# Optimization experiments

Measured on AMD Instinct MI355X. Metric: run time of the kernel, lower is better.

The kernel has to match this reference:

```python
import jax, jax.numpy as jnp
import numpy as np

N_HEADS, HEAD_D, N_LVL, N_PTS, EMB = 8, 32, 1, 4, 256


def _grid_sample(img, grid):
    """Bilinear grid_sample, align_corners=False, zeros padding.
    img: [N,C,H,W], grid: [N,Hg,Wg,2] in [-1,1] (x=width, y=height)."""
    N, C, H, W = img.shape
    x = (grid[..., 0] + 1.0) * (W * 0.5) - 0.5
    y = (grid[..., 1] + 1.0) * (H * 0.5) - 0.5
    x0 = jnp.floor(x); y0 = jnp.floor(y)
    x1 = x0 + 1.0; y1 = y0 + 1.0
    wx1 = x - x0; wx0 = 1.0 - wx1
    wy1 = y - y0; wy0 = 1.0 - wy1
    img_flat = img.reshape(N, C, H * W)

    def gather(xi, yi, w):
        xii = xi.astype(jnp.int32); yii = yi.astype(jnp.int32)
        valid = (xii >= 0) & (xii < W) & (yii >= 0) & (yii < H)
        lin = jnp.clip(yii, 0, H - 1) * W + jnp.clip(xii, 0, W - 1)   # [N,Hg,Wg]
        vals = jnp.take_along_axis(img_flat, lin.reshape(N, 1, -1), axis=2)
        vals = vals.reshape(N, C, lin.shape[1], lin.shape[2])
        return vals * (w * valid)[:, None]

    return (gather(x0, y0, wx0 * wy0) + gather(x1, y0, wx1 * wy0)
            + gather(x0, y1, wx0 * wy1) + gather(x1, y1, wx1 * wy1))


def setup_inputs() -> dict:
    key = jax.random.key(0)
    ks = jax.random.split(key, 16)
    bs, nq, Hl, Wl = 4, 10000, 100, 100
    nv = Hl * Wl
    s = 0.02
    return {
        "query": jax.random.normal(ks[0], (bs, nq, EMB), jnp.float32),
        "key": jax.random.normal(ks[1], (bs, nv, EMB), jnp.float32),
        "value": jax.random.normal(ks[2], (bs, nv, EMB), jnp.float32),
        "reference_points": jax.random.uniform(ks[3], (bs, nq, N_LVL, 2), jnp.float32),
        "Wq": s * jax.random.normal(ks[4], (HEAD_D, HEAD_D), jnp.float32),
        "bq": jnp.zeros((HEAD_D,), jnp.float32),
        "Wk": s * jax.random.normal(ks[5], (HEAD_D, HEAD_D), jnp.float32),
        "bk": jnp.zeros((HEAD_D,), jnp.float32),
        "Wv": s * jax.random.normal(ks[6], (HEAD_D, HEAD_D), jnp.float32),
        "bv": jnp.zeros((HEAD_D,), jnp.float32),
        "Woff": s * jax.random.normal(ks[7], (N_LVL * N_PTS * 2, HEAD_D), jnp.float32),
        "boff": jnp.zeros((N_LVL * N_PTS * 2,), jnp.float32),
        "Wo": s * jax.random.normal(ks[8], (EMB, EMB), jnp.float32),
        "bo": jnp.zeros((EMB,), jnp.float32),
        "spatial_shapes": jnp.array([[Hl, Wl]], dtype=jnp.int32),
    }


def reference(query, key, value, reference_points, Wq, bq, Wk, bk, Wv, bv,
              Woff, boff, Wo, bo, spatial_shapes):
    nH, D, nL, nP = N_HEADS, HEAD_D, N_LVL, N_PTS
    bs, nq, _ = query.shape
    ss = np.asarray(spatial_shapes)                      # static [L,2] (H,W)
    residual = query
    qh = query.reshape(bs, nq, nH, D)
    kh = key.reshape(bs, -1, nH, D)
    vh = value.reshape(bs, -1, nH, D)
    norm = jnp.asarray(np.stack([ss[:, 1], ss[:, 0]], -1), jnp.float32)  # (W,H) per level
    off = (qh @ Woff.T + boff).reshape(bs, nq, nH, nL, nP, 2)
    loc = reference_points[:, :, None, :, None, :] + off / norm[None, None, None, :, None, :]
    grids = 2.0 * loc - 1.0                              # [b,q,h,L,P,2]
    k_parts, v_parts = [], []
    start = 0
    for l in range(nL):
        Hl, Wl = int(ss[l, 0]), int(ss[l, 1])
        sl = slice(start, start + Hl * Wl); start += Hl * Wl
        k_img = kh[:, sl].reshape(bs, Hl * Wl, nH * D).transpose(0, 2, 1).reshape(bs * nH, D, Hl, Wl)
        v_img = vh[:, sl].reshape(bs, Hl * Wl, nH * D).transpose(0, 2, 1).reshape(bs * nH, D, Hl, Wl)
        # NOTE: key grid uses only the FIRST query's sampling locations (as in source: grids[:, :1])
        gk = grids[:, :1, :, l].transpose(0, 2, 1, 3, 4).reshape(bs * nH, 1, nP, 2)
        gv = grids[:, :, :, l].transpose(0, 2, 1, 3, 4).reshape(bs * nH, nq, nP, 2)
        k_parts.append(_grid_sample(k_img, gk))          # [bH, D, 1, P]
        v_parts.append(_grid_sample(v_img, gv))          # [bH, D, nq, P]
    k_samp = jnp.stack(k_parts, axis=-2).reshape(bs * nH, D, nL * nP)
    k_samp = k_samp.reshape(bs, nH, D, nL * nP).transpose(0, 3, 1, 2)     # [b, LP, h, d]
    v_samp = jnp.stack(v_parts, axis=-2).reshape(bs * nH, D, nq, nL * nP)  # [bH, d, q, LP]
    q = qh @ Wq.T + bq                                                    # [b, q, h, d]
    k = k_samp @ Wk.T + bk                                                # [b, LP, h, d]
    v = (v_samp.transpose(0, 2, 3, 1) @ Wv.T + bv).transpose(0, 3, 1, 2)  # [bH, d, q, LP]
    attn = jax.nn.softmax(jnp.einsum('bqhd,bkhd->bqhk', q, k), axis=-1)   # [b, q, h, LP]
    attn = attn.transpose(0, 2, 1, 3).reshape(bs * nH, 1, nq, nL * nP)
    out = (v * attn).sum(-1).reshape(bs, nH * D, nq).transpose(0, 2, 1)   # [b, q, E]
    return out @ Wo.T + bo + residual  # dropout is identity in eval mode
```

## Files before the change

### kernel.cpp

```cpp
#include <hip/hip_runtime.h>
#include <hip/hip_bf16.h>
#include <math.h>

#define NH   8
#define HD   32
#define NP   4
#define EMB  256
#define IMG_H 100
#define IMG_W 100
#define NQ   10000
#define NV   10000
#define BS   4

#define W4S 36

#define FENCE() asm volatile("" ::: "memory")

typedef __attribute__((ext_vector_type(8))) short bf16x8;
typedef __attribute__((ext_vector_type(4))) float f32x4;

#define KT_OFF    0
#define KB_OFF    16384
#define BO2_OFF   17408
#define WCF_OFF   18432
#define WCB_OFF   (18432 + 262144)
#define PREB_OFF  (18432 + 262144 + 131072)
#define WS_MIN    ((size_t)PREB_OFF)
#define WS_FULL   ((size_t)PREB_OFF + (size_t)BS * NQ * EMB * 2)

__global__ __launch_bounds__(64) void k1_keys(
    const float* __restrict__ query, const float* __restrict__ key,
    const float* __restrict__ refp,  const float* __restrict__ Woff,
    const float* __restrict__ boff,  const float* __restrict__ Wk,
    const float* __restrict__ bk,    const float* __restrict__ Wq,
    const float* __restrict__ bq,
    float* __restrict__ kt, float* __restrict__ kb)
{
    int b = blockIdx.x >> 3, h = blockIdx.x & 7;
    __shared__ float q0[HD];
    __shared__ float off[8];
    __shared__ float ks[NP][HD];
    __shared__ float kkl[NP][HD];
    int l = threadIdx.x;

    if (l < HD) q0[l] = query[(size_t)(b * NQ) * EMB + h * HD + l];
    __syncthreads();

    if (l < 8) {
        float s = boff[l];
        #pragma unroll
        for (int d = 0; d < HD; ++d) s += q0[d] * Woff[l * HD + d];
        off[l] = s;
    }
    __syncthreads();

    if (l < HD) {
        float refx = refp[(size_t)(b * NQ) * 2 + 0];
        float refy = refp[(size_t)(b * NQ) * 2 + 1];
        for (int p = 0; p < NP; ++p) {
            float x = refx * IMG_W + off[p * 2 + 0] - 0.5f;
            float y = refy * IMG_H + off[p * 2 + 1] - 0.5f;
            float x0f = floorf(x), y0f = floorf(y);
            int ix0 = (int)x0f, iy0 = (int)y0f;
            float fx = x - x0f, fy = y - y0f;
            float acc = 0.f;
            #pragma unroll
            for (int cy = 0; cy < 2; ++cy)
                #pragma unroll
                for (int cx = 0; cx < 2; ++cx) {
                    int xi = ix0 + cx, yi = iy0 + cy;
                    if ((unsigned)xi < IMG_W && (unsigned)yi < IMG_H) {
                        float wgt = (cx ? fx : 1.f - fx) * (cy ? fy : 1.f - fy);
                        acc += wgt * key[((size_t)b * NV + yi * IMG_W + xi) * EMB + h * HD + l];
                    }
                }
            ks[p][l] = acc;
        }
    }
    __syncthreads();

    #pragma unroll
    for (int t = 0; t < 2; ++t) {
        int idx = l + 64 * t;
        int p = idx >> 5, dout = idx & 31;
        float s = bk[dout];
        #pragma unroll
        for (int d = 0; d < HD; ++d) s += Wk[dout * HD + d] * ks[p][d];
        kkl[p][dout] = s;
    }
    __syncthreads();

    #pragma unroll
    for (int t = 0; t < 2; ++t) {
        int idx = l + 64 * t;
        int p = idx >> 5, d = idx & 31;
        float s = 0.f;
        #pragma unroll
        for (int dd = 0; dd < HD; ++dd) s += Wq[dd * HD + d] * kkl[p][dd];
        kt[((b * NP + p) * NH + h) * HD + d] = s;
    }
    if (l < NP) {
        float s = 0.f;
        #pragma unroll
        for (int dd = 0; dd < HD; ++dd) s += bq[dd] * kkl[l][dd];
        kb[(b * NP + l) * NH + h] = s;
    }
}

__global__ __launch_bounds__(256) void kcomb(
    const float* __restrict__ Wo, const float* __restrict__ Wv,
    const float* __restrict__ bv, const float* __restrict__ bo,
    float* __restrict__ wcf, __hip_bfloat16* __restrict__ wcb,
    float* __restrict__ bo2)
{
    __shared__ float sWv[HD * HD];
    __shared__ float sWoR[EMB];
    __shared__ float sws[4];
    int e = blockIdx.x, col = threadIdx.x;
    *(float4*)&sWv[col * 4] = *(const float4*)(Wv + col * 4);
    sWoR[col] = Wo[(size_t)e * EMB + col];
    __syncthreads();

    int h = col >> 5, d = col & 31;
    float s = 0.f;
    #pragma unroll
    for (int dd = 0; dd < HD; ++dd) s += sWoR[h * HD + dd] * sWv[dd * HD + d];
    wcf[(size_t)e * EMB + col] = s;
    wcb[(size_t)e * EMB + col] = __float2bfloat16(s);

    float pb = bv[d] * sWoR[col];
    #pragma unroll
    for (int o = 1; o < 64; o <<= 1) pb += __shfl_xor(pb, o);
    if ((col & 63) == 0) sws[col >> 6] = pb;
    __syncthreads();
    if (col == 0) bo2[e] = bo[e] + sws[0] + sws[1] + sws[2] + sws[3];
}

template<int BF16OUT>
__global__ __launch_bounds__(256) void k2_main(
    const float* __restrict__ query, const float* __restrict__ value,
    const float* __restrict__ refp,
    const float* __restrict__ Woff, const float* __restrict__ boff,
    const float* __restrict__ kt, const float* __restrict__ kb,
    float* __restrict__ pre, __hip_bfloat16* __restrict__ preb)
{
    __shared__ float sWoff[8 * W4S];
    __shared__ float sboff[8];
    __shared__ float skt[NP * NH * W4S];
    __shared__ float skb[NP * NH];
    __shared__ float qld[4][NH * W4S];
    __shared__ float offs[4][64];
    __shared__ float attnw[4][32];
    __shared__ int   soff4[4][32][4];
    __shared__ float swgt4[4][32][4];

    int tid = threadIdx.x;
    int b0 = (blockIdx.x * 4) / NQ;

    for (int i = tid; i < 8 * HD; i += 256) sWoff[(i >> 5) * W4S + (i & 31)] = Woff[i];
    if (tid < 8)  sboff[tid] = boff[tid];
    {
        int j = tid * 4;
        *(float4*)&skt[(j >> 5) * W4S + (j & 31)] =
            *(const float4*)(kt + b0 * (NP * NH * HD) + j);
    }
    if (tid < NP * NH) skb[tid] = kb[b0 * (NP * NH) + tid];

    int w = tid >> 6, lane = tid & 63;
    int gq = blockIdx.x * 4 + w;
    int b = b0;

    float4 qv = *(const float4*)(query + (size_t)gq * EMB + lane * 4);
    { int e = lane * 4; *(float4*)&qld[w][(e >> 5) * W4S + (e & 31)] = qv; }
    float refx = refp[(size_t)gq * 2 + 0];
    float refy = refp[(size_t)gq * 2 + 1];
    __syncthreads();

    int h = lane >> 3, t = lane & 7;

    float qr[HD];
    #pragma unroll
    for (int d = 0; d < HD; d += 4) {
        float4 v4 = *(const float4*)&qld[w][h * W4S + d];
        qr[d] = v4.x; qr[d + 1] = v4.y; qr[d + 2] = v4.z; qr[d + 3] = v4.w;
    }

    {
        float s = sboff[t];
        const float* wr = &sWoff[t * W4S];
        #pragma unroll
        for (int d = 0; d < HD; d += 4) {
            float4 ww = *(const float4*)(wr + d);
            s += qr[d] * ww.x + qr[d+1] * ww.y + qr[d+2] * ww.z + qr[d+3] * ww.w;
        }
        offs[w][h * 8 + t] = s;
    }

    float plog[NP];
    #pragma unroll
    for (int p = 0; p < NP; ++p) {
        const float* kr = &skt[(p * NH + h) * W4S];
        float s = 0.f;
        #pragma unroll
        for (int k = 0; k < 4; ++k) s += qr[t + 8 * k] * kr[t + 8 * k];
        plog[p] = s;
    }
    #pragma unroll
    for (int p = 0; p < NP; ++p) {
        plog[p] += __shfl_xor(plog[p], 1, 8);
        plog[p] += __shfl_xor(plog[p], 2, 8);
        plog[p] += __shfl_xor(plog[p], 4, 8);
        plog[p] += skb[p * NH + h];
    }
    {
        float mm = fmaxf(fmaxf(plog[0], plog[1]), fmaxf(plog[2], plog[3]));
        float e0 = __expf(plog[0] - mm), e1 = __expf(plog[1] - mm);
        float e2 = __expf(plog[2] - mm), e3 = __expf(plog[3] - mm);
        float inv = 1.f / (e0 + e1 + e2 + e3);
        if (t < 4) {
            float a = (t == 0) ? e0 : (t == 1) ? e1 : (t == 2) ? e2 : e3;
            attnw[w][h * 4 + t] = a * inv;
        }
    }
    FENCE();

    if (lane < 32) {
        int h2 = lane >> 2, p = lane & 3;
        float x = refx * IMG_W + offs[w][h2 * 8 + p * 2 + 0] - 0.5f;
        float y = refy * IMG_H + offs[w][h2 * 8 + p * 2 + 1] - 0.5f;
        float x0f = floorf(x), y0f = floorf(y);
        int ix0 = (int)x0f, iy0 = (int)y0f;
        float fx = x - x0f, fy = y - y0f;
        float aw = attnw[w][lane];
        float wx1 = fx * aw, wx0 = aw - wx1;
        int bbase = b * (NV * EMB) + h2 * HD;
        int   o4[4]; float g4[4];
        #pragma unroll
        for (int c = 0; c < 4; ++c) {
            int cx = c & 1, cy = c >> 1;
            int xi = ix0 + cx, yi = iy0 + cy;
            bool valid = ((unsigned)xi < IMG_W) & ((unsigned)yi < IMG_H);
            int xc = min(max(xi, 0), IMG_W - 1);
            int yc = min(max(yi, 0), IMG_H - 1);
            o4[c] = bbase + (yc * IMG_W + xc) * EMB;
            float wv = (cx ? wx1 : wx0) * (cy ? fy : 1.f - fy);
            g4[c] = valid ? wv : 0.f;
        }
        int4   ov = {o4[0], o4[1], o4[2], o4[3]};
        float4 gv = {g4[0], g4[1], g4[2], g4[3]};
        *(int4*)&soff4[w][lane][0]   = ov;
        *(float4*)&swgt4[w][lane][0] = gv;
    }
    FENCE();

    {
        int half = lane >> 5, dcol = lane & 31;
        #pragma unroll
        for (int i = 0; i < 4; ++i) {
            int hh = i * 2 + half;
            float vals[16], wv[16];
            #pragma unroll
            for (int p = 0; p < NP; ++p) {
                int hp = hh * 4 + p;
                int4   o4 = *(const int4*)&soff4[w][hp][0];
                float4 g4 = *(const float4*)&swgt4[w][hp][0];
                vals[p*4+0] = value[(unsigned)(o4.x + dcol)];
                vals[p*4+1] = value[(unsigned)(o4.y + dcol)];
                vals[p*4+2] = value[(unsigned)(o4.z + dcol)];
                vals[p*4+3] = value[(unsigned)(o4.w + dcol)];
                wv[p*4+0] = g4.x; wv[p*4+1] = g4.y; wv[p*4+2] = g4.z; wv[p*4+3] = g4.w;
            }
            float acc = 0.f;
            #pragma unroll
            for (int u = 0; u < 16; ++u) acc += wv[u] * vals[u];
            if (BF16OUT)
                preb[(size_t)gq * EMB + hh * HD + dcol] = __float2bfloat16(acc);
            else
                pre[(size_t)gq * EMB + hh * HD + dcol] = acc;
        }
    }
}

__global__ __launch_bounds__(256) void k3_mfma(
    const __hip_bfloat16* __restrict__ preb, const __hip_bfloat16* __restrict__ wcb,
    float* __restrict__ outp, const float* __restrict__ query,
    const float* __restrict__ bo2)
{
    int w = threadIdx.x >> 6, lane = threadIdx.x & 63;
    size_t m0 = (size_t)blockIdx.x * 64;
    int n0 = w * 64;
    int lr = lane & 15, lg = lane >> 4;

    const short* pa = (const short*)preb;
    const short* pb = (const short*)wcb;

    f32x4 acc[4][4];
    #pragma unroll
    for (int mt = 0; mt < 4; ++mt)
        #pragma unroll
        for (int nt = 0; nt < 4; ++nt) acc[mt][nt] = (f32x4){0.f, 0.f, 0.f, 0.f};

    #pragma unroll
    for (int k0 = 0; k0 < EMB; k0 += 32) {
        bf16x8 af[4], bf[4];
        #pragma unroll
        for (int mt = 0; mt < 4; ++mt)
            af[mt] = *(const bf16x8*)(pa + (m0 + mt * 16 + lr) * EMB + k0 + lg * 8);
        #pragma unroll
        for (int nt = 0; nt < 4; ++nt)
            bf[nt] = *(const bf16x8*)(pb + (size_t)(n0 + nt * 16 + lr) * EMB + k0 + lg * 8);
        #pragma unroll
        for (int mt = 0; mt < 4; ++mt)
            #pragma unroll
            for (int nt = 0; nt < 4; ++nt)
                acc[mt][nt] = __builtin_amdgcn_mfma_f32_16x16x32_bf16(
                    af[mt], bf[nt], acc[mt][nt], 0, 0, 0);
    }

    float bov[4];
    #pragma unroll
    for (int nt = 0; nt < 4; ++nt) bov[nt] = bo2[n0 + nt * 16 + lr];

    #pragma unroll
    for (int mt = 0; mt < 4; ++mt)
        #pragma unroll
        for (int q = 0; q < 4; ++q) {
            size_t row = m0 + mt * 16 + lg * 4 + q;
            const float* qrow = query + row * EMB;
            float* orow = outp + row * EMB;
            #pragma unroll
            for (int nt = 0; nt < 4; ++nt) {
                int col = n0 + nt * 16 + lr;
                orow[col] = acc[mt][nt][q] + bov[nt] + qrow[col];
            }
        }
}

__global__ __launch_bounds__(256) void k3_gemm(
    const float* __restrict__ pre, float* __restrict__ outp,
    const float* __restrict__ query, const float* __restrict__ wcf,
    const float* __restrict__ bo2)
{
    __shared__ float As[64 * EMB];
    int tid = threadIdx.x;
    size_t r0 = (size_t)blockIdx.x * 64;
    {
        const float4* src = (const float4*)(pre + r0 * EMB);
        float4* dst = (float4*)As;
        for (int i = tid; i < 64 * EMB / 4; i += 256) dst[i] = src[i];
    }
    __syncthreads();

    int w = tid >> 6, lane = tid & 63;
    int rb = w * 16;
    float acc[16][4];
    #pragma unroll
    for (int r = 0; r < 16; ++r)
        #pragma unroll
        for (int j = 0; j < 4; ++j) acc[r][j] = 0.f;

    for (int kc = 0; kc < EMB / 4; ++kc) {
        float4 wreg[4];
        #pragma unroll
        for (int j = 0; j < 4; ++j)
            wreg[j] = *(const float4*)&wcf[(size_t)(lane + 64 * j) * EMB + kc * 4];
        #pragma unroll
        for (int r = 0; r < 16; ++r) {
            float4 a = *(const float4*)&As[(rb + r) * EMB + kc * 4];
            #pragma unroll
            for (int j = 0; j < 4; ++j)
                acc[r][j] += a.x * wreg[j].x + a.y * wreg[j].y
                           + a.z * wreg[j].z + a.w * wreg[j].w;
        }
    }

    #pragma unroll
    for (int r = 0; r < 16; ++r) {
        size_t row = r0 + rb + r;
        #pragma unroll
        for (int j = 0; j < 4; ++j) {
            int c = lane + 64 * j;
            outp[row * EMB + c] = acc[r][j] + bo2[c] + query[row * EMB + c];
        }
    }
}

extern "C" void kernel_launch(void* const* d_in, const int* in_sizes, int n_in,
                              void* d_out, int out_size, void* d_ws, size_t ws_size,
                              hipStream_t stream) {
    const float* query = (const float*)d_in[0];
    const float* key   = (const float*)d_in[1];
    const float* value = (const float*)d_in[2];
    const float* refp  = (const float*)d_in[3];
    const float* Wq   = (const float*)d_in[4];
    const float* bq   = (const float*)d_in[5];
    const float* Wk   = (const float*)d_in[6];
    const float* bk   = (const float*)d_in[7];
    const float* Wv   = (const float*)d_in[8];
    const float* bv   = (const float*)d_in[9];
    const float* Woff = (const float*)d_in[10];
    const float* boff = (const float*)d_in[11];
    const float* Wo   = (const float*)d_in[12];
    const float* bo   = (const float*)d_in[13];
    (void)in_sizes; (void)n_in; (void)out_size;

    float* out = (float*)d_out;
    char*  ws  = (char*)d_ws;
    float* kt  = (float*)(ws + KT_OFF);
    float* kb  = (float*)(ws + KB_OFF);
    float* bo2 = (float*)(ws + BO2_OFF);
    float* wcf = (float*)(ws + WCF_OFF);
    __hip_bfloat16* wcb = (__hip_bfloat16*)(ws + WCB_OFF);

    k1_keys<<<BS * NH, 64, 0, stream>>>(query, key, refp, Woff, boff, Wk, bk,
                                        Wq, bq, kt, kb);
    kcomb<<<EMB, 256, 0, stream>>>(Wo, Wv, bv, bo, wcf, wcb, bo2);

    if (ws_size >= WS_FULL) {
        __hip_bfloat16* preb = (__hip_bfloat16*)(ws + PREB_OFF);
        k2_main<1><<<BS * NQ / 4, 256, 0, stream>>>(query, value, refp, Woff, boff,
                                                    kt, kb, nullptr, preb);
        k3_mfma<<<BS * NQ / 64, 256, 0, stream>>>(preb, wcb, out, query, bo2);
    } else {
        k2_main<0><<<BS * NQ / 4, 256, 0, stream>>>(query, value, refp, Woff, boff,
                                                    kt, kb, out, nullptr);
        k3_gemm<<<BS * NQ / 64, 256, 0, stream>>>(out, out, query, wcf, bo2);
    }
}
```

Baseline: 93.53 us.

## Fuse sampling and output MFMA GEMM into one kernel via LDS staging

Merges the bilinear-sampling/attention kernel with the bf16 MFMA output projection. Each block handles 32 queries, keeps the aggregated bf16 rows in shared memory and runs the GEMM directly from LDS, so the bf16 intermediate no longer makes a round trip through global memory and one launch is dropped. The value gather now loads float4 per lane instead of scalars, and blocks are remapped across XCDs for locality. In exchange it adds a sequential per-wave loop over 8 queries, more shared memory per block, and only 1252 blocks, which may reduce occupancy and latency hiding for the gathers.

```diff
diff --git a/kernel.cpp b/kernel.cpp
--- a/kernel.cpp
+++ b/kernel.cpp
@@ -13,6 +13,9 @@
 #define BS   4
 
 #define W4S 36
+#define QPB 32
+#define NBLK 313
+#define AGS 264
 
 #define FENCE() asm volatile("" ::: "memory")
 
@@ -24,9 +27,7 @@
 #define BO2_OFF   17408
 #define WCF_OFF   18432
 #define WCB_OFF   (18432 + 262144)
-#define PREB_OFF  (18432 + 262144 + 131072)
-#define WS_MIN    ((size_t)PREB_OFF)
-#define WS_FULL   ((size_t)PREB_OFF + (size_t)BS * NQ * EMB * 2)
+#define WS_FUSED  ((size_t)WCB_OFF + 131072)
 
 __global__ __launch_bounds__(64) void k1_keys(
     const float* __restrict__ query, const float* __restrict__ key,
@@ -126,7 +127,7 @@
     #pragma unroll
     for (int dd = 0; dd < HD; ++dd) s += sWoR[h * HD + dd] * sWv[dd * HD + d];
     wcf[(size_t)e * EMB + col] = s;
-    wcb[(size_t)e * EMB + col] = __float2bfloat16(s);
+    if (wcb) wcb[(size_t)e * EMB + col] = __float2bfloat16(s);
 
     float pb = bv[d] * sWoR[col];
     #pragma unroll
@@ -136,23 +137,228 @@
     if (col == 0) bo2[e] = bo[e] + sws[0] + sws[1] + sws[2] + sws[3];
 }
 
-template<int BF16OUT>
-__global__ __launch_bounds__(256) void k2_main(
+__global__ __launch_bounds__(256) void k2f(
     const float* __restrict__ query, const float* __restrict__ value,
     const float* __restrict__ refp,
     const float* __restrict__ Woff, const float* __restrict__ boff,
     const float* __restrict__ kt, const float* __restrict__ kb,
-    float* __restrict__ pre, __hip_bfloat16* __restrict__ preb)
+    const __hip_bfloat16* __restrict__ wcb, const float* __restrict__ bo2,
+    float* __restrict__ outp)
 {
     __shared__ float sWoff[8 * W4S];
     __shared__ float sboff[8];
     __shared__ float skt[NP * NH * W4S];
     __shared__ float skb[NP * NH];
-    __shared__ float qld[4][NH * W4S];
     __shared__ float offs[4][64];
     __shared__ float attnw[4][32];
     __shared__ int   soff4[4][32][4];
     __shared__ float swgt4[4][32][4];
+    __shared__ __hip_bfloat16 agg[QPB][AGS];
+
+    int tid = threadIdx.x;
+
+    const int nwg = BS * NBLK;
+    int bid = blockIdx.x;
+    int xcd = bid & 7, idx = bid >> 3;
+    const int qch = nwg >> 3, rch = nwg & 7;
+    int wg = (xcd < rch) ? xcd * (qch + 1) + idx
+                         : rch * (qch + 1) + (xcd - rch) * qch + idx;
+    int b = wg / NBLK;
+    int blk = wg - b * NBLK;
+    int qbase = blk * QPB;
+    int nvalid = NQ - qbase; if (nvalid > QPB) nvalid = QPB;
+
+    for (int i = tid; i < 8 * HD; i += 256) sWoff[(i >> 5) * W4S + (i & 31)] = Woff[i];
+    if (tid < 8) sboff[tid] = boff[tid];
+    {
+        int j = tid * 4;
+        *(float4*)&skt[(j >> 5) * W4S + (j & 31)] =
+            *(const float4*)(kt + b * (NP * NH * HD) + j);
+    }
+    if (tid < NP * NH) skb[tid] = kb[b * (NP * NH) + tid];
+    __syncthreads();
+
+    int w = tid >> 6, lane = tid & 63;
+    int h = lane >> 3, t = lane & 7;
+
+    for (int qi = 0; qi < 8; ++qi) {
+        int lq = w * 8 + qi;
+        if (lq < nvalid) {
+            int gq = b * NQ + qbase + lq;
+
+            float qr[HD];
+            const float* qrow = query + (size_t)gq * EMB + h * HD;
+            #pragma unroll
+            for (int d = 0; d < HD; d += 4) {
+                float4 v4 = *(const float4*)(qrow + d);
+                qr[d] = v4.x; qr[d+1] = v4.y; qr[d+2] = v4.z; qr[d+3] = v4.w;
+            }
+            float refx = refp[(size_t)gq * 2 + 0];
+            float refy = refp[(size_t)gq * 2 + 1];
+
+            {
+                float s = sboff[t];
+                const float* wr = &sWoff[t * W4S];
+                #pragma unroll
+                for (int d = 0; d < HD; d += 4) {
+                    float4 ww = *(const float4*)(wr + d);
+                    s += qr[d]*ww.x + qr[d+1]*ww.y + qr[d+2]*ww.z + qr[d+3]*ww.w;
+                }
+                offs[w][h * 8 + t] = s;
+            }
+
+            float plog[NP];
+            #pragma unroll
+            for (int p = 0; p < NP; ++p) {
+                const float* kr = &skt[(p * NH + h) * W4S];
+                float s = 0.f;
+                #pragma unroll
+                for (int k = 0; k < 4; ++k) s += qr[t + 8 * k] * kr[t + 8 * k];
+                plog[p] = s;
+            }
+            #pragma unroll
+            for (int p = 0; p < NP; ++p) {
+                plog[p] += __shfl_xor(plog[p], 1, 8);
+                plog[p] += __shfl_xor(plog[p], 2, 8);
+                plog[p] += __shfl_xor(plog[p], 4, 8);
+                plog[p] += skb[p * NH + h];
+            }
+            {
+                float mm = fmaxf(fmaxf(plog[0], plog[1]), fmaxf(plog[2], plog[3]));
+                float e0 = __expf(plog[0]-mm), e1 = __expf(plog[1]-mm);
+                float e2 = __expf(plog[2]-mm), e3 = __expf(plog[3]-mm);
+                float inv = 1.f / (e0 + e1 + e2 + e3);
+                if (t < 4) {
+                    float a = (t == 0) ? e0 : (t == 1) ? e1 : (t == 2) ? e2 : e3;
+                    attnw[w][h * 4 + t] = a * inv;
+                }
+            }
+            FENCE();
+
+            if (lane < 32) {
+                int h2 = lane >> 2, p = lane & 3;
+                float x = refx * IMG_W + offs[w][h2 * 8 + p * 2 + 0] - 0.5f;
+                float y = refy * IMG_H + offs[w][h2 * 8 + p * 2 + 1] - 0.5f;
+                float x0f = floorf(x), y0f = floorf(y);
+                int ix0 = (int)x0f, iy0 = (int)y0f;
+                float fx = x - x0f, fy = y - y0f;
+                float aw = attnw[w][lane];
+                float wx1 = fx * aw, wx0 = aw - wx1;
+                int bbase = b * (NV * EMB) + h2 * HD;
+                int   o4[4]; float g4[4];
+                #pragma unroll
+                for (int c = 0; c < 4; ++c) {
+                    int cx = c & 1, cy = c >> 1;
+                    int xi = ix0 + cx, yi = iy0 + cy;
+                    bool valid = ((unsigned)xi < IMG_W) & ((unsigned)yi < IMG_H);
+                    int xc = min(max(xi, 0), IMG_W - 1);
+                    int yc = min(max(yi, 0), IMG_H - 1);
+                    o4[c] = (bbase + (yc * IMG_W + xc) * EMB) * 4;
+                    float wv = (cx ? wx1 : wx0) * (cy ? fy : 1.f - fy);
+                    g4[c] = valid ? wv : 0.f;
+                }
+                int4   ov = {o4[0], o4[1], o4[2], o4[3]};
+                float4 gv = {g4[0], g4[1], g4[2], g4[3]};
+                *(int4*)&soff4[w][lane][0]   = ov;
+                *(float4*)&swgt4[w][lane][0] = gv;
+            }
+            FENCE();
+
+            {
+                unsigned co = t * 16;
+                const char* vb = (const char*)value;
+                float4 acc = {0.f, 0.f, 0.f, 0.f};
+                #pragma unroll
+                for (int p = 0; p < NP; ++p) {
+                    int hp = h * 4 + p;
+                    int4   o4 = *(const int4*)&soff4[w][hp][0];
+                    float4 g4 = *(const float4*)&swgt4[w][hp][0];
+                    float4 v0 = *(const float4*)(vb + (unsigned)o4.x + co);
+                    float4 v1 = *(const float4*)(vb + (unsigned)o4.y + co);
+                    float4 v2 = *(const float4*)(vb + (unsigned)o4.z + co);
+                    float4 v3 = *(const float4*)(vb + (unsigned)o4.w + co);
+                    acc.x += g4.x*v0.x + g4.y*v1.x + g4.z*v2.x + g4.w*v3.x;
+                    acc.y += g4.x*v0.y + g4.y*v1.y + g4.z*v2.y + g4.w*v3.y;
+                    acc.z += g4.x*v0.z + g4.y*v1.z + g4.z*v2.z + g4.w*v3.z;
+                    acc.w += g4.x*v0.w + g4.y*v1.w + g4.z*v2.w + g4.w*v3.w;
+                }
+                __hip_bfloat16 pk[4];
+                pk[0] = __float2bfloat16(acc.x);
+                pk[1] = __float2bfloat16(acc.y);
+                pk[2] = __float2bfloat16(acc.z);
+                pk[3] = __float2bfloat16(acc.w);
+                *(ushort4*)&agg[lq][h * HD + t * 4] = *(const ushort4*)&pk[0];
+            }
+        }
+    }
+    __syncthreads();
+
+    {
+        int lr = lane & 15, lg = lane >> 4;
+        int n0 = w * 64;
+        const short* pb = (const short*)wcb;
+
+        f32x4 acc[2][4];
+        #pragma unroll
+        for (int mt = 0; mt < 2; ++mt)
+            #pragma unroll
+            for (int nt = 0; nt < 4; ++nt) acc[mt][nt] = (f32x4){0.f,0.f,0.f,0.f};
+
+        #pragma unroll
+        for (int k0 = 0; k0 < EMB; k0 += 32) {
+            bf16x8 af[2], bf[4];
+            #pragma unroll
+            for (int mt = 0; mt < 2; ++mt)
+                af[mt] = *(const bf16x8*)&agg[mt * 16 + lr][k0 + lg * 8];
+            #pragma unroll
+            for (int nt = 0; nt < 4; ++nt)
+                bf[nt] = *(const bf16x8*)(pb + (size_t)(n0 + nt*16 + lr) * EMB + k0 + lg*8);
+            #pragma unroll
+            for (int mt = 0; mt < 2; ++mt)
+                #pragma unroll
+                for (int nt = 0; nt < 4; ++nt)
+                    acc[mt][nt] = __builtin_amdgcn_mfma_f32_16x16x32_bf16(
+                        af[mt], bf[nt], acc[mt][nt], 0, 0, 0);
+        }
+
+        float bov[4];
+        #pragma unroll
+        for (int nt = 0; nt < 4; ++nt) bov[nt] = bo2[n0 + nt * 16 + lr];
+
+        #pragma unroll
+        for (int mt = 0; mt < 2; ++mt)
+            #pragma unroll
+            for (int q2 = 0; q2 < 4; ++q2) {
+                int m = mt * 16 + lg * 4 + q2;
+                if (m < nvalid) {
+                    size_t row = (size_t)b * NQ + qbase + m;
+                    const float* qrw = query + row * EMB;
+                    float* orow = outp + row * EMB;
+                    #pragma unroll
+                    for (int nt = 0; nt < 4; ++nt) {
+                        int col = n0 + nt * 16 + lr;
+                        orow[col] = acc[mt][nt][q2] + bov[nt] + qrw[col];
+                    }
+                }
+            }
+    }
+}
+
+__global__ __launch_bounds__(256) void k2_plain(
+    const float* __restrict__ query, const float* __restrict__ value,
+    const float* __restrict__ refp,
+    const float* __restrict__ Woff, const float* __restrict__ boff,
+    const float* __restrict__ kt, const float* __restrict__ kb,
+    float* __restrict__ pre)
+{
+    __shared__ float sWoff[8 * W4S];
+    __shared__ float sboff[8];
+    __shared__ float skt[NP * NH * W4S];
+    __shared__ float skb[NP * NH];
+    __shared__ float offs[4][64];
+    __shared__ float attnw[4][32];
+    __shared__ int   soff4[4][32][4];
+    __shared__ float swgt4[4][32][4];
 
     int tid = threadIdx.x;
     int b0 = (blockIdx.x * 4) / NQ;
@@ -165,25 +371,21 @@
             *(const float4*)(kt + b0 * (NP * NH * HD) + j);
     }
     if (tid < NP * NH) skb[tid] = kb[b0 * (NP * NH) + tid];
+    __syncthreads();
 
     int w = tid >> 6, lane = tid & 63;
     int gq = blockIdx.x * 4 + w;
-    int b = b0;
-
-    float4 qv = *(const float4*)(query + (size_t)gq * EMB + lane * 4);
-    { int e = lane * 4; *(float4*)&qld[w][(e >> 5) * W4S + (e & 31)] = qv; }
+    int h = lane >> 3, t = lane & 7;
+
+    float qr[HD];
+    const float* qrow = query + (size_t)gq * EMB + h * HD;
+    #pragma unroll
+    for (int d = 0; d < HD; d += 4) {
+        float4 v4 = *(const float4*)(qrow + d);
+        qr[d] = v4.x; qr[d+1] = v4.y; qr[d+2] = v4.z; qr[d+3] = v4.w;
+    }
     float refx = refp[(size_t)gq * 2 + 0];
     float refy = refp[(size_t)gq * 2 + 1];
-    __syncthreads();
-
-    int h = lane >> 3, t = lane & 7;
-
-    float qr[HD];
-    #pragma unroll
-    for (int d = 0; d < HD; d += 4) {
-        float4 v4 = *(const float4*)&qld[w][h * W4S + d];
-        qr[d] = v4.x; qr[d + 1] = v4.y; qr[d + 2] = v4.z; qr[d + 3] = v4.w;
-    }
 
     {
         float s = sboff[t];
@@ -191,11 +393,10 @@
         #pragma unroll
         for (int d = 0; d < HD; d += 4) {
             float4 ww = *(const float4*)(wr + d);
-            s += qr[d] * ww.x + qr[d+1] * ww.y + qr[d+2] * ww.z + qr[d+3] * ww.w;
+            s += qr[d]*ww.x + qr[d+1]*ww.y + qr[d+2]*ww.z + qr[d+3]*ww.w;
         }
         offs[w][h * 8 + t] = s;
     }
-
     float plog[NP];
     #pragma unroll
     for (int p = 0; p < NP; ++p) {
@@ -214,8 +415,8 @@
     }
     {
         float mm = fmaxf(fmaxf(plog[0], plog[1]), fmaxf(plog[2], plog[3]));
-        float e0 = __expf(plog[0] - mm), e1 = __expf(plog[1] - mm);
-        float e2 = __expf(plog[2] - mm), e3 = __expf(plog[3] - mm);
+        float e0 = __expf(plog[0]-mm), e1 = __expf(plog[1]-mm);
+        float e2 = __expf(plog[2]-mm), e3 = __expf(plog[3]-mm);
         float inv = 1.f / (e0 + e1 + e2 + e3);
         if (t < 4) {
             float a = (t == 0) ? e0 : (t == 1) ? e1 : (t == 2) ? e2 : e3;
@@ -223,7 +424,6 @@
         }
     }
     FENCE();
-
     if (lane < 32) {
         int h2 = lane >> 2, p = lane & 3;
         float x = refx * IMG_W + offs[w][h2 * 8 + p * 2 + 0] - 0.5f;
@@ -233,7 +433,7 @@
         float fx = x - x0f, fy = y - y0f;
         float aw = attnw[w][lane];
         float wx1 = fx * aw, wx0 = aw - wx1;
-        int bbase = b * (NV * EMB) + h2 * HD;
+        int bbase = b0 * (NV * EMB) + h2 * HD;
         int   o4[4]; float g4[4];
         #pragma unroll
         for (int c = 0; c < 4; ++c) {
@@ -242,7 +442,7 @@
             bool valid = ((unsigned)xi < IMG_W) & ((unsigned)yi < IMG_H);
             int xc = min(max(xi, 0), IMG_W - 1);
             int yc = min(max(yi, 0), IMG_H - 1);
-            o4[c] = bbase + (yc * IMG_W + xc) * EMB;
+            o4[c] = (bbase + (yc * IMG_W + xc) * EMB) * 4;
             float wv = (cx ? wx1 : wx0) * (cy ? fy : 1.f - fy);
             g4[c] = valid ? wv : 0.f;
         }
@@ -252,88 +452,26 @@
         *(float4*)&swgt4[w][lane][0] = gv;
     }
     FENCE();
-
-    {
-        int half = lane >> 5, dcol = lane & 31;
-        #pragma unroll
-        for (int i = 0; i < 4; ++i) {
-            int hh = i * 2 + half;
-            float vals[16], wv[16];
-            #pragma unroll
-            for (int p = 0; p < NP; ++p) {
-                int hp = hh * 4 + p;
-                int4   o4 = *(const int4*)&soff4[w][hp][0];
-                float4 g4 = *(const float4*)&swgt4[w][hp][0];
-                vals[p*4+0] = value[(unsigned)(o4.x + dcol)];
-                vals[p*4+1] = value[(unsigned)(o4.y + dcol)];
-                vals[p*4+2] = value[(unsigned)(o4.z + dcol)];
-                vals[p*4+3] = value[(unsigned)(o4.w + dcol)];
-                wv[p*4+0] = g4.x; wv[p*4+1] = g4.y; wv[p*4+2] = g4.z; wv[p*4+3] = g4.w;
-            }
-            float acc = 0.f;
-            #pragma unroll
-            for (int u = 0; u < 16; ++u) acc += wv[u] * vals[u];
-            if (BF16OUT)
-                preb[(size_t)gq * EMB + hh * HD + dcol] = __float2bfloat16(acc);
-            else
-                pre[(size_t)gq * EMB + hh * HD + dcol] = acc;
-        }
-    }
-}
-
-__global__ __launch_bounds__(256) void k3_mfma(
-    const __hip_bfloat16* __restrict__ preb, const __hip_bfloat16* __restrict__ wcb,
-    float* __restrict__ outp, const float* __restrict__ query,
-    const float* __restrict__ bo2)
-{
-    int w = threadIdx.x >> 6, lane = threadIdx.x & 63;
-    size_t m0 = (size_t)blockIdx.x * 64;
-    int n0 = w * 64;
-    int lr = lane & 15, lg = lane >> 4;
-
-    const short* pa = (const short*)preb;
-    const short* pb = (const short*)wcb;
-
-    f32x4 acc[4][4];
-    #pragma unroll
-    for (int mt = 0; mt < 4; ++mt)
-        #pragma unroll
-        for (int nt = 0; nt < 4; ++nt) acc[mt][nt] = (f32x4){0.f, 0.f, 0.f, 0.f};
-
-    #pragma unroll
-    for (int k0 = 0; k0 < EMB; k0 += 32) {
-        bf16x8 af[4], bf[4];
-        #pragma unroll
-        for (int mt = 0; mt < 4; ++mt)
-            af[mt] = *(const bf16x8*)(pa + (m0 + mt * 16 + lr) * EMB + k0 + lg * 8);
-        #pragma unroll
-        for (int nt = 0; nt < 4; ++nt)
-            bf[nt] = *(const bf16x8*)(pb + (size_t)(n0 + nt * 16 + lr) * EMB + k0 + lg * 8);
-        #pragma unroll
-        for (int mt = 0; mt < 4; ++mt)
-            #pragma unroll
-            for (int nt = 0; nt < 4; ++nt)
-                acc[mt][nt] = __builtin_amdgcn_mfma_f32_16x16x32_bf16(
-                    af[mt], bf[nt], acc[mt][nt], 0, 0, 0);
-    }
-
-    float bov[4];
-    #pragma unroll
-    for (int nt = 0; nt < 4; ++nt) bov[nt] = bo2[n0 + nt * 16 + lr];
-
-    #pragma unroll
-    for (int mt = 0; mt < 4; ++mt)
-        #pragma unroll
-        for (int q = 0; q < 4; ++q) {
-            size_t row = m0 + mt * 16 + lg * 4 + q;
-            const float* qrow = query + row * EMB;
-            float* orow = outp + row * EMB;
-            #pragma unroll
-            for (int nt = 0; nt < 4; ++nt) {
-                int col = n0 + nt * 16 + lr;
-                orow[col] = acc[mt][nt][q] + bov[nt] + qrow[col];
-            }
-        }
+    {
+        unsigned co = t * 16;
+        const char* vb = (const char*)value;
+        float4 acc = {0.f, 0.f, 0.f, 0.f};
+        #pragma unroll
+        for (int p = 0; p < NP; ++p) {
+            int hp = h * 4 + p;
+            int4   o4 = *(const int4*)&soff4[w][hp][0];
+            float4 g4 = *(const float4*)&swgt4[w][hp][0];
+            float4 v0 = *(const float4*)(vb + (unsigned)o4.x + co);
+            float4 v1 = *(const float4*)(vb + (unsigned)o4.y + co);
+            float4 v2 = *(const float4*)(vb + (unsigned)o4.z + co);
+            float4 v3 = *(const float4*)(vb + (unsigned)o4.w + co);
+            acc.x += g4.x*v0.x + g4.y*v1.x + g4.z*v2.x + g4.w*v3.x;
+            acc.y += g4.x*v0.y + g4.y*v1.y + g4.z*v2.y + g4.w*v3.y;
+            acc.z += g4.x*v0.z + g4.y*v1.z + g4.z*v2.z + g4.w*v3.z;
+            acc.w += g4.x*v0.w + g4.y*v1.w + g4.z*v2.w + g4.w*v3.w;
+        }
+        *(float4*)(pre + (size_t)gq * EMB + h * HD + t * 4) = acc;
+    }
 }
 
 __global__ __launch_bounds__(256) void k3_gemm(
@@ -410,20 +548,19 @@
     float* kb  = (float*)(ws + KB_OFF);
     float* bo2 = (float*)(ws + BO2_OFF);
     float* wcf = (float*)(ws + WCF_OFF);
-    __hip_bfloat16* wcb = (__hip_bfloat16*)(ws + WCB_OFF);
+    __hip_bfloat16* wcb = (ws_size >= WS_FUSED) ? (__hip_bfloat16*)(ws + WCB_OFF)
+                                                : nullptr;
 
     k1_keys<<<BS * NH, 64, 0, stream>>>(query, key, refp, Woff, boff, Wk, bk,
                                         Wq, bq, kt, kb);
     kcomb<<<EMB, 256, 0, stream>>>(Wo, Wv, bv, bo, wcf, wcb, bo2);
 
-    if (ws_size >= WS_FULL) {
-        __hip_bfloat16* preb = (__hip_bfloat16*)(ws + PREB_OFF);
-        k2_main<1><<<BS * NQ / 4, 256, 0, stream>>>(query, value, refp, Woff, boff,
-                                                    kt, kb, nullptr, preb);
-        k3_mfma<<<BS * NQ / 64, 256, 0, stream>>>(preb, wcb, out, query, bo2);
+    if (ws_size >= WS_FUSED) {
+        k2f<<<BS * NBLK, 256, 0, stream>>>(query, value, refp, Woff, boff,
+                                           kt, kb, wcb, bo2, out);
     } else {
-        k2_main<0><<<BS * NQ / 4, 256, 0, stream>>>(query, value, refp, Woff, boff,
-                                                    kt, kb, out, nullptr);
+        k2_plain<<<BS * NQ / 4, 256, 0, stream>>>(query, value, refp, Woff, boff,
+                                                  kt, kb, out);
         k3_gemm<<<BS * NQ / 64, 256, 0, stream>>>(out, out, query, wcf, bo2);
     }
 }
```

Result: slower. 97.75 us (+4.5%).

## Gather value rows once over a shared 3x3 pixel window per query

Applied to the files above, without the earlier changes.

Sampling offsets are small, so all 32 head/point samples of a query usually land in a 3x3 pixel window around the reference point. The kernel now accumulates the bilinear and attention weights per head into nine window slots using shared-memory atomics. It then reads nine full 256-float value rows with float4 loads, instead of sixteen scattered scalar loads per output element. If any sample falls outside the window, the wave falls back to a per-sample float4 gather. This adds atomics and a wave-wide ballot, and the fast path only pays off when offsets stay small, which depends on the input data.

```diff
diff --git a/kernel.cpp b/kernel.cpp
--- a/kernel.cpp
+++ b/kernel.cpp
@@ -25,7 +25,6 @@
 #define WCF_OFF   18432
 #define WCB_OFF   (18432 + 262144)
 #define PREB_OFF  (18432 + 262144 + 131072)
-#define WS_MIN    ((size_t)PREB_OFF)
 #define WS_FULL   ((size_t)PREB_OFF + (size_t)BS * NQ * EMB * 2)
 
 __global__ __launch_bounds__(64) void k1_keys(
@@ -126,7 +125,7 @@
     #pragma unroll
     for (int dd = 0; dd < HD; ++dd) s += sWoR[h * HD + dd] * sWv[dd * HD + d];
     wcf[(size_t)e * EMB + col] = s;
-    wcb[(size_t)e * EMB + col] = __float2bfloat16(s);
+    if (wcb) wcb[(size_t)e * EMB + col] = __float2bfloat16(s);
 
     float pb = bv[d] * sWoR[col];
     #pragma unroll
@@ -137,7 +136,7 @@
 }
 
 template<int BF16OUT>
-__global__ __launch_bounds__(256) void k2_main(
+__global__ __launch_bounds__(256) void k2w(
     const float* __restrict__ query, const float* __restrict__ value,
     const float* __restrict__ refp,
     const float* __restrict__ Woff, const float* __restrict__ boff,
@@ -151,8 +150,8 @@
     __shared__ float qld[4][NH * W4S];
     __shared__ float offs[4][64];
     __shared__ float attnw[4][32];
-    __shared__ int   soff4[4][32][4];
-    __shared__ float swgt4[4][32][4];
+    __shared__ float coefL[4][96];
+    __shared__ int   winaddr[4][12];
 
     int tid = threadIdx.x;
     int b0 = (blockIdx.x * 4) / NQ;
@@ -191,7 +190,7 @@
         #pragma unroll
         for (int d = 0; d < HD; d += 4) {
             float4 ww = *(const float4*)(wr + d);
-            s += qr[d] * ww.x + qr[d+1] * ww.y + qr[d+2] * ww.z + qr[d+3] * ww.w;
+            s += qr[d]*ww.x + qr[d+1]*ww.y + qr[d+2]*ww.z + qr[d+3]*ww.w;
         }
         offs[w][h * 8 + t] = s;
     }
@@ -214,8 +213,8 @@
     }
     {
         float mm = fmaxf(fmaxf(plog[0], plog[1]), fmaxf(plog[2], plog[3]));
-        float e0 = __expf(plog[0] - mm), e1 = __expf(plog[1] - mm);
-        float e2 = __expf(plog[2] - mm), e3 = __expf(plog[3] - mm);
+        float e0 = __expf(plog[0]-mm), e1 = __expf(plog[1]-mm);
+        float e2 = __expf(plog[2]-mm), e3 = __expf(plog[3]-mm);
         float inv = 1.f / (e0 + e1 + e2 + e3);
         if (t < 4) {
             float a = (t == 0) ? e0 : (t == 1) ? e1 : (t == 2) ? e2 : e3;
@@ -224,59 +223,109 @@
     }
     FENCE();
 
+    float xr = refx * IMG_W - 0.5f;
+    float yr = refy * IMG_H - 0.5f;
+    int rcx = (int)floorf(xr + 0.5f);
+    int rcy = (int)floorf(yr + 0.5f);
+
+    {
+        coefL[w][lane] = 0.f;
+        if (lane < 32) coefL[w][64 + lane] = 0.f;
+    }
+    if (lane < 9) {
+        int i = lane % 3, j = lane / 3;
+        int xc = min(max(rcx - 1 + i, 0), IMG_W - 1);
+        int yc = min(max(rcy - 1 + j, 0), IMG_H - 1);
+        winaddr[w][lane] = (b * (NV * EMB) + (yc * IMG_W + xc) * EMB) * 4;
+    }
+    FENCE();
+
+    bool inwin = true;
     if (lane < 32) {
         int h2 = lane >> 2, p = lane & 3;
         float x = refx * IMG_W + offs[w][h2 * 8 + p * 2 + 0] - 0.5f;
         float y = refy * IMG_H + offs[w][h2 * 8 + p * 2 + 1] - 0.5f;
         float x0f = floorf(x), y0f = floorf(y);
         int ix0 = (int)x0f, iy0 = (int)y0f;
-        float fx = x - x0f, fy = y - y0f;
-        float aw = attnw[w][lane];
-        float wx1 = fx * aw, wx0 = aw - wx1;
-        int bbase = b * (NV * EMB) + h2 * HD;
-        int   o4[4]; float g4[4];
-        #pragma unroll
-        for (int c = 0; c < 4; ++c) {
-            int cx = c & 1, cy = c >> 1;
-            int xi = ix0 + cx, yi = iy0 + cy;
-            bool valid = ((unsigned)xi < IMG_W) & ((unsigned)yi < IMG_H);
-            int xc = min(max(xi, 0), IMG_W - 1);
-            int yc = min(max(yi, 0), IMG_H - 1);
-            o4[c] = bbase + (yc * IMG_W + xc) * EMB;
-            float wv = (cx ? wx1 : wx0) * (cy ? fy : 1.f - fy);
-            g4[c] = valid ? wv : 0.f;
-        }
-        int4   ov = {o4[0], o4[1], o4[2], o4[3]};
-        float4 gv = {g4[0], g4[1], g4[2], g4[3]};
-        *(int4*)&soff4[w][lane][0]   = ov;
-        *(float4*)&swgt4[w][lane][0] = gv;
-    }
+        int dx0 = ix0 - (rcx - 1), dy0 = iy0 - (rcy - 1);
+        inwin = ((unsigned)dx0 <= 1u) & ((unsigned)dy0 <= 1u);
+        if (inwin) {
+            float fx = x - x0f, fy = y - y0f;
+            float aw = attnw[w][lane];
+            float wx1 = fx * aw, wx0 = aw - wx1;
+            #pragma unroll
+            for (int c = 0; c < 4; ++c) {
+                int cx = c & 1, cy = c >> 1;
+                int xi = ix0 + cx, yi = iy0 + cy;
+                bool valid = ((unsigned)xi < IMG_W) & ((unsigned)yi < IMG_H);
+                float g = (cx ? wx1 : wx0) * (cy ? fy : 1.f - fy);
+                g = valid ? g : 0.f;
+                int slot = (dy0 + cy) * 3 + (dx0 + cx);
+                atomicAdd(&coefL[w][h2 * 12 + slot], g);
+            }
+        }
+    }
+    unsigned long long obal = __ballot(!inwin);
     FENCE();
 
-    {
-        int half = lane >> 5, dcol = lane & 31;
-        #pragma unroll
-        for (int i = 0; i < 4; ++i) {
-            int hh = i * 2 + half;
-            float vals[16], wv[16];
-            #pragma unroll
-            for (int p = 0; p < NP; ++p) {
-                int hp = hh * 4 + p;
-                int4   o4 = *(const int4*)&soff4[w][hp][0];
-                float4 g4 = *(const float4*)&swgt4[w][hp][0];
-                vals[p*4+0] = value[(unsigned)(o4.x + dcol)];
-                vals[p*4+1] = value[(unsigned)(o4.y + dcol)];
-                vals[p*4+2] = value[(unsigned)(o4.z + dcol)];
-                vals[p*4+3] = value[(unsigned)(o4.w + dcol)];
-                wv[p*4+0] = g4.x; wv[p*4+1] = g4.y; wv[p*4+2] = g4.z; wv[p*4+3] = g4.w;
+    float4 acc = {0.f, 0.f, 0.f, 0.f};
+    if (obal == 0ULL) {
+        int wa[9];
+        #pragma unroll
+        for (int r = 0; r < 9; ++r) wa[r] = winaddr[w][r];
+        float cf[9];
+        #pragma unroll
+        for (int r = 0; r < 9; ++r) cf[r] = coefL[w][h * 12 + r];
+        const char* vb = (const char*)value;
+        unsigned lo = (unsigned)(lane * 16);
+        #pragma unroll
+        for (int r = 0; r < 9; ++r) {
+            float4 v = *(const float4*)(vb + (unsigned)wa[r] + lo);
+            acc.x += cf[r] * v.x; acc.y += cf[r] * v.y;
+            acc.z += cf[r] * v.z; acc.w += cf[r] * v.w;
+        }
+    } else {
+        unsigned co = (unsigned)((lane & 7) * 16);
+        const char* vb = (const char*)value;
+        #pragma unroll
+        for (int p = 0; p < NP; ++p) {
+            float x = refx * IMG_W + offs[w][h * 8 + p * 2 + 0] - 0.5f;
+            float y = refy * IMG_H + offs[w][h * 8 + p * 2 + 1] - 0.5f;
+            float x0f = floorf(x), y0f = floorf(y);
+            int ix0 = (int)x0f, iy0 = (int)y0f;
+            float fx = x - x0f, fy = y - y0f;
+            float aw = attnw[w][h * 4 + p];
+            float wx1 = fx * aw, wx0 = aw - wx1;
+            #pragma unroll
+            for (int c = 0; c < 4; ++c) {
+                int cx = c & 1, cy = c >> 1;
+                int xi = ix0 + cx, yi = iy0 + cy;
+                bool valid = ((unsigned)xi < IMG_W) & ((unsigned)yi < IMG_H);
+                int xc = min(max(xi, 0), IMG_W - 1);
+                int yc = min(max(yi, 0), IMG_H - 1);
+                float g = (cx ? wx1 : wx0) * (cy ? fy : 1.f - fy);
+                g = valid ? g : 0.f;
+                unsigned addr = (unsigned)((b * (NV * EMB)
+                              + (yc * IMG_W + xc) * EMB + h * HD) * 4) + co;
+                float4 v = *(const float4*)(vb + addr);
+                acc.x += g * v.x; acc.y += g * v.y;
+                acc.z += g * v.z; acc.w += g * v.w;
             }
-            float acc = 0.f;
-            #pragma unroll
-            for (int u = 0; u < 16; ++u) acc += wv[u] * vals[u];
-            if (BF16OUT)
-                preb[(size_t)gq * EMB + hh * HD + dcol] = __float2bfloat16(acc);
-            else
-                pre[(size_t)gq * EMB + hh * HD + dcol] = acc;
+        }
+    }
+
+    {
+        int cb = (lane & 7) * 4;
+        if (BF16OUT) {
+            __hip_bfloat16 pk[4];
+            pk[0] = __float2bfloat16(acc.x);
+            pk[1] = __float2bfloat16(acc.y);
+            pk[2] = __float2bfloat16(acc.z);
+            pk[3] = __float2bfloat16(acc.w);
+            *(ushort4*)((unsigned short*)preb + (size_t)gq * EMB + h * HD + cb) =
+                *(const ushort4*)&pk[0];
+        } else {
+            *(float4*)(pre + (size_t)gq * EMB + h * HD + cb) = acc;
         }
     }
 }
@@ -418,12 +467,12 @@
 
     if (ws_size >= WS_FULL) {
         __hip_bfloat16* preb = (__hip_bfloat16*)(ws + PREB_OFF);
-        k2_main<1><<<BS * NQ / 4, 256, 0, stream>>>(query, value, refp, Woff, boff,
-                                                    kt, kb, nullptr, preb);
+        k2w<1><<<BS * NQ / 4, 256, 0, stream>>>(query, value, refp, Woff, boff,
+                                                kt, kb, nullptr, preb);
         k3_mfma<<<BS * NQ / 64, 256, 0, stream>>>(preb, wcb, out, query, bo2);
     } else {
-        k2_main<0><<<BS * NQ / 4, 256, 0, stream>>>(query, value, refp, Woff, boff,
-                                                    kt, kb, out, nullptr);
+        k2w<0><<<BS * NQ / 4, 256, 0, stream>>>(query, value, refp, Woff, boff,
+                                                kt, kb, out, nullptr);
         k3_gemm<<<BS * NQ / 64, 256, 0, stream>>>(out, out, query, wcf, bo2);
     }
 }
```

After: 107.4 us. 14.9% more time.

## Bucket-sort queries by reference tile and vectorize bilinear value gather

Applied to the files above, without the earlier changes.

Adds a counting sort (count, scan, scatter kernels) that groups queries by the 2x2 spatial tile of their reference point. The main sampling kernel then visits queries in that order, so neighbouring workgroups gather overlapping value rows and get more cache reuse. Block indices are also swizzled across groups of eight, and each lane now gathers a float4 of channels through byte offsets instead of scalar loads. The cost is three extra small kernel launches, a memset, one more indirection per query, and atomics in the sort.

```diff
diff --git a/kernel.cpp b/kernel.cpp
--- a/kernel.cpp
+++ b/kernel.cpp
@@ -13,6 +13,9 @@
 #define BS   4
 
 #define W4S 36
+#define TS  2
+#define TPL (IMG_W / TS)
+#define TPB (TPL * TPL)
 
 #define FENCE() asm volatile("" ::: "memory")
 
@@ -24,8 +27,11 @@
 #define BO2_OFF   17408
 #define WCF_OFF   18432
 #define WCB_OFF   (18432 + 262144)
-#define PREB_OFF  (18432 + 262144 + 131072)
-#define WS_MIN    ((size_t)PREB_OFF)
+#define CNT_OFF   (WCB_OFF + 131072)
+#define OFF_OFF   (CNT_OFF + 40000)
+#define QIDX_OFF  (OFF_OFF + 40000)
+#define PREB_OFF  ((QIDX_OFF + 160000 + 63) & ~63ULL)
+#define WS_SORT   ((size_t)QIDX_OFF + 160000)
 #define WS_FULL   ((size_t)PREB_OFF + (size_t)BS * NQ * EMB * 2)
 
 __global__ __launch_bounds__(64) void k1_keys(
@@ -126,7 +132,7 @@
     #pragma unroll
     for (int dd = 0; dd < HD; ++dd) s += sWoR[h * HD + dd] * sWv[dd * HD + d];
     wcf[(size_t)e * EMB + col] = s;
-    wcb[(size_t)e * EMB + col] = __float2bfloat16(s);
+    if (wcb) wcb[(size_t)e * EMB + col] = __float2bfloat16(s);
 
     float pb = bv[d] * sWoR[col];
     #pragma unroll
@@ -136,12 +142,69 @@
     if (col == 0) bo2[e] = bo[e] + sws[0] + sws[1] + sws[2] + sws[3];
 }
 
+__device__ __forceinline__ int tile_of(const float* refp, int gq) {
+    float rx = refp[(size_t)gq * 2 + 0];
+    float ry = refp[(size_t)gq * 2 + 1];
+    int px = min(max((int)(rx * IMG_W), 0), IMG_W - 1);
+    int py = min(max((int)(ry * IMG_H), 0), IMG_H - 1);
+    return (py / TS) * TPL + (px / TS);
+}
+
+__global__ __launch_bounds__(256) void ksort_count(
+    const float* __restrict__ refp, int* __restrict__ cnt)
+{
+    int gq = blockIdx.x * 256 + threadIdx.x;
+    if (gq < BS * NQ) {
+        int b = gq / NQ;
+        atomicAdd(&cnt[b * TPB + tile_of(refp, gq)], 1);
+    }
+}
+
+__global__ __launch_bounds__(64) void ksort_scan(
+    const int* __restrict__ cnt, int* __restrict__ off)
+{
+    int b = blockIdx.x, lane = threadIdx.x;
+    const int PER = (TPB + 63) / 64;
+    int lsum[PER];
+    int s = 0;
+    #pragma unroll
+    for (int i = 0; i < PER; ++i) {
+        int t = lane * PER + i;
+        int c = (t < TPB) ? cnt[b * TPB + t] : 0;
+        lsum[i] = s; s += c;
+    }
+    int inc = s;
+    #pragma unroll
+    for (int o = 1; o < 64; o <<= 1) {
+        int v = __shfl_up(inc, o);
+        if (lane >= o) inc += v;
+    }
+    int excl = inc - s;
+    #pragma unroll
+    for (int i = 0; i < PER; ++i) {
+        int t = lane * PER + i;
+        if (t < TPB) off[b * TPB + t] = b * NQ + excl + lsum[i];
+    }
+}
+
+__global__ __launch_bounds__(256) void ksort_scatter(
+    const float* __restrict__ refp, int* __restrict__ off, int* __restrict__ qidx)
+{
+    int gq = blockIdx.x * 256 + threadIdx.x;
+    if (gq < BS * NQ) {
+        int b = gq / NQ;
+        int slot = atomicAdd(&off[b * TPB + tile_of(refp, gq)], 1);
+        qidx[slot] = gq;
+    }
+}
+
 template<int BF16OUT>
-__global__ __launch_bounds__(256) void k2_main(
+__global__ __launch_bounds__(256) void k2s(
     const float* __restrict__ query, const float* __restrict__ value,
     const float* __restrict__ refp,
     const float* __restrict__ Woff, const float* __restrict__ boff,
     const float* __restrict__ kt, const float* __restrict__ kb,
+    const int* __restrict__ qidx,
     float* __restrict__ pre, __hip_bfloat16* __restrict__ preb)
 {
     __shared__ float sWoff[8 * W4S];
@@ -155,7 +218,10 @@
     __shared__ float swgt4[4][32][4];
 
     int tid = threadIdx.x;
-    int b0 = (blockIdx.x * 4) / NQ;
+
+    int bid = blockIdx.x;
+    int wg = (bid & 7) * (BS * NQ / 4 / 8) + (bid >> 3);
+    int b0 = (wg * 4) / NQ;
 
     for (int i = tid; i < 8 * HD; i += 256) sWoff[(i >> 5) * W4S + (i & 31)] = Woff[i];
     if (tid < 8)  sboff[tid] = boff[tid];
@@ -167,7 +233,7 @@
     if (tid < NP * NH) skb[tid] = kb[b0 * (NP * NH) + tid];
 
     int w = tid >> 6, lane = tid & 63;
-    int gq = blockIdx.x * 4 + w;
+    int gq = qidx ? qidx[wg * 4 + w] : (wg * 4 + w);
     int b = b0;
 
     float4 qv = *(const float4*)(query + (size_t)gq * EMB + lane * 4);
@@ -191,7 +257,7 @@
         #pragma unroll
         for (int d = 0; d < HD; d += 4) {
             float4 ww = *(const float4*)(wr + d);
-            s += qr[d] * ww.x + qr[d+1] * ww.y + qr[d+2] * ww.z + qr[d+3] * ww.w;
+            s += qr[d]*ww.x + qr[d+1]*ww.y + qr[d+2]*ww.z + qr[d+3]*ww.w;
         }
         offs[w][h * 8 + t] = s;
     }
@@ -214,8 +280,8 @@
     }
     {
         float mm = fmaxf(fmaxf(plog[0], plog[1]), fmaxf(plog[2], plog[3]));
-        float e0 = __expf(plog[0] - mm), e1 = __expf(plog[1] - mm);
-        float e2 = __expf(plog[2] - mm), e3 = __expf(plog[3] - mm);
+        float e0 = __expf(plog[0]-mm), e1 = __expf(plog[1]-mm);
+        float e2 = __expf(plog[2]-mm), e3 = __expf(plog[3]-mm);
         float inv = 1.f / (e0 + e1 + e2 + e3);
         if (t < 4) {
             float a = (t == 0) ? e0 : (t == 1) ? e1 : (t == 2) ? e2 : e3;
@@ -242,7 +308,7 @@
             bool valid = ((unsigned)xi < IMG_W) & ((unsigned)yi < IMG_H);
             int xc = min(max(xi, 0), IMG_W - 1);
             int yc = min(max(yi, 0), IMG_H - 1);
-            o4[c] = bbase + (yc * IMG_W + xc) * EMB;
+            o4[c] = (bbase + (yc * IMG_W + xc) * EMB) * 4;
             float wv = (cx ? wx1 : wx0) * (cy ? fy : 1.f - fy);
             g4[c] = valid ? wv : 0.f;
         }
@@ -254,29 +320,34 @@
     FENCE();
 
     {
-        int half = lane >> 5, dcol = lane & 31;
-        #pragma unroll
-        for (int i = 0; i < 4; ++i) {
-            int hh = i * 2 + half;
-            float vals[16], wv[16];
-            #pragma unroll
-            for (int p = 0; p < NP; ++p) {
-                int hp = hh * 4 + p;
-                int4   o4 = *(const int4*)&soff4[w][hp][0];
-                float4 g4 = *(const float4*)&swgt4[w][hp][0];
-                vals[p*4+0] = value[(unsigned)(o4.x + dcol)];
-                vals[p*4+1] = value[(unsigned)(o4.y + dcol)];
-                vals[p*4+2] = value[(unsigned)(o4.z + dcol)];
-                vals[p*4+3] = value[(unsigned)(o4.w + dcol)];
-                wv[p*4+0] = g4.x; wv[p*4+1] = g4.y; wv[p*4+2] = g4.z; wv[p*4+3] = g4.w;
-            }
-            float acc = 0.f;
-            #pragma unroll
-            for (int u = 0; u < 16; ++u) acc += wv[u] * vals[u];
-            if (BF16OUT)
-                preb[(size_t)gq * EMB + hh * HD + dcol] = __float2bfloat16(acc);
-            else
-                pre[(size_t)gq * EMB + hh * HD + dcol] = acc;
+        unsigned co = t * 16;
+        const char* vb = (const char*)value;
+        float4 acc = {0.f, 0.f, 0.f, 0.f};
+        #pragma unroll
+        for (int p = 0; p < NP; ++p) {
+            int hp = h * 4 + p;
+            int4   o4 = *(const int4*)&soff4[w][hp][0];
+            float4 g4 = *(const float4*)&swgt4[w][hp][0];
+            float4 v0 = *(const float4*)(vb + (unsigned)o4.x + co);
+            float4 v1 = *(const float4*)(vb + (unsigned)o4.y + co);
+            float4 v2 = *(const float4*)(vb + (unsigned)o4.z + co);
+            float4 v3 = *(const float4*)(vb + (unsigned)o4.w + co);
+            acc.x += g4.x*v0.x + g4.y*v1.x + g4.z*v2.x + g4.w*v3.x;
+            acc.y += g4.x*v0.y + g4.y*v1.y + g4.z*v2.y + g4.w*v3.y;
+            acc.z += g4.x*v0.z + g4.y*v1.z + g4.z*v2.z + g4.w*v3.z;
+            acc.w += g4.x*v0.w + g4.y*v1.w + g4.z*v2.w + g4.w*v3.w;
+        }
+        int cb = t * 4;
+        if (BF16OUT) {
+            __hip_bfloat16 pk[4];
+            pk[0] = __float2bfloat16(acc.x);
+            pk[1] = __float2bfloat16(acc.y);
+            pk[2] = __float2bfloat16(acc.z);
+            pk[3] = __float2bfloat16(acc.w);
+            *(ushort4*)((unsigned short*)preb + (size_t)gq * EMB + h * HD + cb) =
+                *(const ushort4*)&pk[0];
+        } else {
+            *(float4*)(pre + (size_t)gq * EMB + h * HD + cb) = acc;
         }
     }
 }
@@ -412,18 +483,32 @@
     float* wcf = (float*)(ws + WCF_OFF);
     __hip_bfloat16* wcb = (__hip_bfloat16*)(ws + WCB_OFF);
 
+    bool have_sort = (ws_size >= WS_SORT);
+    int* cnt  = (int*)(ws + CNT_OFF);
+    int* off  = (int*)(ws + OFF_OFF);
+    int* qidx = have_sort ? (int*)(ws + QIDX_OFF) : nullptr;
+
+    if (have_sort) hipMemsetAsync(cnt, 0, BS * TPB * sizeof(int), stream);
+
     k1_keys<<<BS * NH, 64, 0, stream>>>(query, key, refp, Woff, boff, Wk, bk,
                                         Wq, bq, kt, kb);
     kcomb<<<EMB, 256, 0, stream>>>(Wo, Wv, bv, bo, wcf, wcb, bo2);
 
+    if (have_sort) {
+        int nthr = (BS * NQ + 255) / 256;
+        ksort_count<<<nthr, 256, 0, stream>>>(refp, cnt);
+        ksort_scan<<<BS, 64, 0, stream>>>(cnt, off);
+        ksort_scatter<<<nthr, 256, 0, stream>>>(refp, off, qidx);
+    }
+
     if (ws_size >= WS_FULL) {
         __hip_bfloat16* preb = (__hip_bfloat16*)(ws + PREB_OFF);
-        k2_main<1><<<BS * NQ / 4, 256, 0, stream>>>(query, value, refp, Woff, boff,
-                                                    kt, kb, nullptr, preb);
+        k2s<1><<<BS * NQ / 4, 256, 0, stream>>>(query, value, refp, Woff, boff,
+                                                kt, kb, qidx, nullptr, preb);
         k3_mfma<<<BS * NQ / 64, 256, 0, stream>>>(preb, wcb, out, query, bo2);
     } else {
-        k2_main<0><<<BS * NQ / 4, 256, 0, stream>>>(query, value, refp, Woff, boff,
-                                                    kt, kb, out, nullptr);
+        k2s<0><<<BS * NQ / 4, 256, 0, stream>>>(query, value, refp, Woff, boff,
+                                                kt, kb, qidx, out, nullptr);
         k3_gemm<<<BS * NQ / 64, 256, 0, stream>>>(out, out, query, wcf, bo2);
     }
 }
```

After: 101.2 us. 1.08x slower.
